# Kernel optimization log

Measured on AMD Instinct MI355X. Metric: run time of the kernel, lower is better.

## Reference

```python
import jax, jax.numpy as jnp
import numpy as np

B, T, E, WIN, OC, VOCAB = 256, 2048, 128, 5, 128, 50000


def setup_inputs() -> dict:
    key = jax.random.key(0)
    k1, k2, k3, k4, k5, k6 = jax.random.split(key, 6)
    return {
        "x": jax.random.randint(k1, (B, T), 0, VOCAB + 1, dtype=jnp.int32),
        "emb_table": jax.random.normal(k2, (VOCAB + 1, E), dtype=jnp.float32),
        "att_w": jax.random.normal(k3, (WIN, E), dtype=jnp.float32) * 0.05,
        "att_b": jax.random.normal(k4, (1,), dtype=jnp.float32),
        "cnn_w": jax.random.normal(k5, (OC, E), dtype=jnp.float32) * 0.05,
        "cnn_b": jax.random.normal(k6, (OC,), dtype=jnp.float32),
    }


def reference(x, emb_table, att_w, att_b, cnn_w, cnn_b):
    win = att_w.shape[0]
    pad = (win - 1) // 2
    embed = emb_table[x]                                   # [B, T, E]
    x_pad = jnp.pad(embed, ((0, 0), (pad, pad), (0, 0)))
    T_ = embed.shape[1]
    # Sliding-window dot product over full embed dim (the degenerate Conv2d)
    s = jnp.zeros(embed.shape[:2], dtype=embed.dtype)      # [B, T]
    for k in range(win):
        s = s + jnp.einsum('bte,e->bt', x_pad[:, k:k + T_, :], att_w[k])
    scores = jax.nn.sigmoid(s + att_b[0])                  # [B, T]
    gated = embed * scores[:, :, None]                     # [B, T, E]
    feat = jnp.tanh(jnp.einsum('bte,oe->bto', gated, cnn_w) + cnn_b)  # [B, T, OC]
    out = jnp.max(feat, axis=1)                            # [B, OC] (maxpool over seq)
    return out[:, :, None, None]                           # [B, OC, 1, 1]
```

## Files before the change

kernel.cpp:

```cpp
#include <hip/hip_runtime.h>
#include <hip/hip_bf16.h>
#include <math.h>

#define B_   256
#define T_   2048
#define E_   128
#define WIN_ 5
#define PAD_ 2
#define OC_  128
#define VOCAB_MAX 50000
#define VOCAB1 50001
#define TT   64
#define REAL_ROWS (TT + WIN_ - 1)
#define ROWS 80
#define ASTR 136
#define VROWS 64

typedef __attribute__((ext_vector_type(8))) short short8;
typedef __attribute__((ext_vector_type(4))) float floatx4;
typedef __attribute__((ext_vector_type(4))) unsigned uintx4;

static __device__ __forceinline__ short f2bf(float f) {
    union { __hip_bfloat16 h; short s; } u;
    u.h = __float2bfloat16(f);
    return u.s;
}

__device__ __forceinline__ void atomicMaxFloat(float* addr, float v) {
    if (v >= 0.0f) atomicMax((int*)addr, __float_as_int(v));
    else           atomicMin((unsigned int*)addr, __float_as_uint(v));
}

__launch_bounds__(256, 4)
__global__ void build_tables(const float* __restrict__ emb,
                             const float* __restrict__ cnn_w,
                             const float* __restrict__ att_w,
                             short* __restrict__ D,
                             float* __restrict__ r,
                             float* __restrict__ out) {
    __shared__ short sh_a[VROWS * ASTR];

    const int tid  = threadIdx.x;
    const int lane = tid & 63;
    const int w    = tid >> 6;
    const int l15  = lane & 15;
    const int quad = lane >> 4;
    const int v0   = blockIdx.x * VROWS;

    if (blockIdx.x < (B_ * OC_) / 256)
        out[blockIdx.x * 256 + tid] = -INFINITY;

    #pragma unroll
    for (int t = 0; t < 8; t++) {
        int i   = t * 256 + tid;
        int row = i >> 5, c4 = i & 31;
        int vr  = v0 + row; if (vr > VOCAB_MAX) vr = VOCAB_MAX;
        float4 v = *(const float4*)(emb + (size_t)vr * E_ + c4 * 4);
        short4 o; o.x = f2bf(v.x); o.y = f2bf(v.y); o.z = f2bf(v.z); o.w = f2bf(v.w);
        *(short4*)(&sh_a[row * ASTR + c4 * 4]) = o;
    }

    short8 Bf[2][4];
    #pragma unroll
    for (int j = 0; j < 2; j++)
        #pragma unroll
        for (int ks = 0; ks < 4; ks++) {
            const float4* p = (const float4*)(cnn_w + (size_t)(w * 32 + j * 16 + l15) * E_ + ks * 32 + quad * 8);
            float4 p0 = p[0], p1 = p[1];
            Bf[j][ks] = (short8){ f2bf(p0.x), f2bf(p0.y), f2bf(p0.z), f2bf(p0.w),
                                  f2bf(p1.x), f2bf(p1.y), f2bf(p1.z), f2bf(p1.w) };
        }

    short8 Ba[4];
    #pragma unroll
    for (int ks = 0; ks < 4; ks++) {
        short8 v = (short8){0,0,0,0,0,0,0,0};
        if (l15 < WIN_) {
            const float4* p = (const float4*)(att_w + (size_t)l15 * E_ + ks * 32 + quad * 8);
            float4 p0 = p[0], p1 = p[1];
            v = (short8){ f2bf(p0.x), f2bf(p0.y), f2bf(p0.z), f2bf(p0.w),
                          f2bf(p1.x), f2bf(p1.y), f2bf(p1.z), f2bf(p1.w) };
        }
        Ba[ks] = v;
    }
    __syncthreads();

    #pragma unroll
    for (int mt = 0; mt < 4; mt++) {
        short8 a[4];
        #pragma unroll
        for (int ks = 0; ks < 4; ks++)
            a[ks] = *(const short8*)(&sh_a[(mt * 16 + l15) * ASTR + ks * 32 + quad * 8]);
        #pragma unroll
        for (int j = 0; j < 2; j++) {
            floatx4 acc = (floatx4){0.f, 0.f, 0.f, 0.f};
            #pragma unroll
            for (int ks = 0; ks < 4; ks++)
                acc = __builtin_amdgcn_mfma_f32_16x16x32_bf16(a[ks], Bf[j][ks], acc, 0, 0, 0);
            #pragma unroll
            for (int rr = 0; rr < 4; rr++) {
                int v = v0 + mt * 16 + quad * 4 + rr;
                if (v <= VOCAB_MAX)
                    D[(size_t)v * E_ + w * 32 + j * 16 + l15] = f2bf(acc[rr]);
            }
        }
    }

    {
        short8 a[4];
        #pragma unroll
        for (int ks = 0; ks < 4; ks++)
            a[ks] = *(const short8*)(&sh_a[(w * 16 + l15) * ASTR + ks * 32 + quad * 8]);
        floatx4 acc = (floatx4){0.f, 0.f, 0.f, 0.f};
        #pragma unroll
        for (int ks = 0; ks < 4; ks++)
            acc = __builtin_amdgcn_mfma_f32_16x16x32_bf16(a[ks], Ba[ks], acc, 0, 0, 0);
        if (l15 < 8) {
            #pragma unroll
            for (int rr = 0; rr < 4; rr++) {
                int v = v0 + w * 16 + quad * 4 + rr;
                if (v <= VOCAB_MAX) r[(size_t)v * 8 + l15] = acc[rr];
            }
        }
    }
}

__launch_bounds__(256, 8)
__global__ void score_max(const int* __restrict__ x,
                          const short* __restrict__ D,
                          const float* __restrict__ r,
                          const float* __restrict__ att_b_p,
                          const float* __restrict__ cnn_b,
                          float* __restrict__ out) {
    __shared__ int   sh_x[260];
    __shared__ float sh_sc[256];
    __shared__ float sh_red[4][128];

    const int tid  = threadIdx.x;
    const int lane = tid & 63;
    const int w    = tid >> 6;
    const int b    = blockIdx.y;
    const int t0   = blockIdx.x * 256;
    const int l15  = lane & 15;
    const int grp  = lane >> 4;

    for (int i = tid; i < 260; i += 256) {
        int t = t0 + i - PAD_;
        sh_x[i] = (t >= 0 && t < T_) ? x[b * T_ + t] : -1;
    }
    __syncthreads();

    {
        float s = att_b_p[0];
        #pragma unroll
        for (int k = 0; k < WIN_; k++) {
            int v = sh_x[tid + k];
            if (v >= 0) s += r[(size_t)v * 8 + k];
        }
        sh_sc[tid] = 1.0f / (1.0f + __expf(-s));
    }
    __syncthreads();

    float mm[8];
    #pragma unroll
    for (int c = 0; c < 8; c++) mm[c] = -INFINITY;

    const int base_t = w * 64;
    for (int i0 = 0; i0 < 64; i0 += 16) {
        uintx4 u[4];
        float  sc4[4];
        #pragma unroll
        for (int j = 0; j < 4; j++) {
            int tok = base_t + i0 + j * 4 + grp;
            int v   = sh_x[tok + PAD_];
            sc4[j]  = sh_sc[tok];
            u[j]    = *(const uintx4*)(D + (size_t)v * E_ + l15 * 8);
        }
        #pragma unroll
        for (int j = 0; j < 4; j++) {
            #pragma unroll
            for (int q = 0; q < 4; q++) {
                float lo = __uint_as_float(u[j][q] << 16);
                float hi = __uint_as_float(u[j][q] & 0xFFFF0000u);
                mm[q * 2]     = fmaxf(mm[q * 2],     sc4[j] * lo);
                mm[q * 2 + 1] = fmaxf(mm[q * 2 + 1], sc4[j] * hi);
            }
        }
    }
    #pragma unroll
    for (int c = 0; c < 8; c++) {
        mm[c] = fmaxf(mm[c], __shfl_xor(mm[c], 16));
        mm[c] = fmaxf(mm[c], __shfl_xor(mm[c], 32));
    }
    if (lane < 16) {
        #pragma unroll
        for (int c = 0; c < 8; c++) sh_red[w][l15 * 8 + c] = mm[c];
    }
    __syncthreads();
    if (tid < 128) {
        float m = fmaxf(fmaxf(sh_red[0][tid], sh_red[1][tid]),
                        fmaxf(sh_red[2][tid], sh_red[3][tid]));
        atomicMaxFloat(&out[b * OC_ + tid], tanhf(m + cnn_b[tid]));
    }
}

__global__ void prep_small(const float* __restrict__ cnn_w, const float* __restrict__ att_w,
                           short* __restrict__ wsw, short* __restrict__ wsatt) {
    int i = blockIdx.x * 256 + threadIdx.x;
    if (i < OC_ * E_)  wsw[i]   = f2bf(cnn_w[i]);
    if (i < WIN_ * E_) wsatt[i] = f2bf(att_w[i]);
}

__launch_bounds__(256, 4)
__global__ void fallback_main(const int* __restrict__ x,
                              const float* __restrict__ emb,
                              const float* __restrict__ att_b_p,
                              const short* __restrict__ wsw,
                              const short* __restrict__ wsatt,
                              const float* __restrict__ cnn_b,
                              float* __restrict__ out) {
    __shared__ short sh_a[ROWS * ASTR];
    __shared__ short sh_att[16 * ASTR];
    __shared__ float sh_r[ROWS * 8];
    __shared__ float sh_score[TT];
    __shared__ int   sh_idx[8 * ROWS];

    const int tid  = threadIdx.x;
    const int lane = tid & 63;
    const int w    = tid >> 6;
    const int b    = blockIdx.y;
    const int t0   = blockIdx.x * (8 * TT);
    const int l15  = lane & 15;
    const int quad = lane >> 4;
    const int rbase = tid >> 4;
    const int c     = tid & 15;

    for (int i = tid; i < 8 * ROWS; i += 256) {
        int tile = i / ROWS, row = i - tile * ROWS;
        int t = t0 + tile * TT + row - PAD_;
        sh_idx[i] = (row < REAL_ROWS && t >= 0 && t < T_) ? x[b * T_ + t] : -1;
    }
    {
        int o = tid >> 4, cc = tid & 15;
        short8 v = (short8){0,0,0,0,0,0,0,0};
        if (o < WIN_) v = *(const short8*)(wsatt + o * E_ + cc * 8);
        *(short8*)(&sh_att[o * ASTR + cc * 8]) = v;
    }
    short8 Bf[2][4];
    #pragma unroll
    for (int j = 0; j < 2; j++)
        #pragma unroll
        for (int ks = 0; ks < 4; ks++)
            Bf[j][ks] = *(const short8*)(wsw + (size_t)(w * 32 + j * 16 + l15) * E_ + ks * 32 + quad * 8);
    __syncthreads();

    short8 g[5];
    #pragma unroll
    for (int k = 0; k < 5; k++) {
        int idx = sh_idx[rbase + 16 * k];
        short8 v = (short8){0,0,0,0,0,0,0,0};
        if (idx >= 0) {
            const float4* p = (const float4*)(emb + (size_t)idx * E_ + c * 8);
            float4 p0 = p[0], p1 = p[1];
            v = (short8){ f2bf(p0.x), f2bf(p0.y), f2bf(p0.z), f2bf(p0.w),
                          f2bf(p1.x), f2bf(p1.y), f2bf(p1.z), f2bf(p1.w) };
        }
        g[k] = v;
    }
    #pragma unroll
    for (int k = 0; k < 5; k++)
        *(short8*)(&sh_a[(rbase + 16 * k) * ASTR + c * 8]) = g[k];
    __syncthreads();

    const float attb = att_b_p[0];
    float mm[2] = { -INFINITY, -INFINITY };

    for (int it = 0; it < 8; it++) {
        for (int mt = w; mt < 5; mt += 4) {
            floatx4 acc = (floatx4){0.f, 0.f, 0.f, 0.f};
            #pragma unroll
            for (int ks = 0; ks < 4; ks++) {
                short8 a  = *(const short8*)(&sh_a[(mt * 16 + l15) * ASTR + ks * 32 + quad * 8]);
                short8 bs = *(const short8*)(&sh_att[l15 * ASTR + ks * 32 + quad * 8]);
                acc = __builtin_amdgcn_mfma_f32_16x16x32_bf16(a, bs, acc, 0, 0, 0);
            }
            if (l15 < 8) {
                #pragma unroll
                for (int r = 0; r < 4; r++)
                    sh_r[(mt * 16 + quad * 4 + r) * 8 + l15] = acc[r];
            }
        }
        __syncthreads();

        if (it + 1 < 8) {
            const int* idxp = &sh_idx[(it + 1) * ROWS];
            #pragma unroll
            for (int k = 0; k < 5; k++) {
                int idx = idxp[rbase + 16 * k];
                short8 v = (short8){0,0,0,0,0,0,0,0};
                if (idx >= 0) {
                    const float4* p = (const float4*)(emb + (size_t)idx * E_ + c * 8);
                    float4 p0 = p[0], p1 = p[1];
                    v = (short8){ f2bf(p0.x), f2bf(p0.y), f2bf(p0.z), f2bf(p0.w),
                                  f2bf(p1.x), f2bf(p1.y), f2bf(p1.z), f2bf(p1.w) };
                }
                g[k] = v;
            }
        }

        if (tid < TT) {
            float s = attb;
            #pragma unroll
            for (int k = 0; k < WIN_; k++) s += sh_r[(tid + k) * 8 + k];
            sh_score[tid] = 1.0f / (1.0f + __expf(-s));
        }

        floatx4 acc[4][2];
        #pragma unroll
        for (int i = 0; i < 4; i++)
            #pragma unroll
            for (int j = 0; j < 2; j++) acc[i][j] = (floatx4){0.f, 0.f, 0.f, 0.f};
        #pragma unroll
        for (int ks = 0; ks < 4; ks++) {
            int ko = ks * 32 + quad * 8;
            #pragma unroll
            for (int i = 0; i < 4; i++) {
                short8 ai = *(const short8*)(&sh_a[(PAD_ + i * 16 + l15) * ASTR + ko]);
                acc[i][0] = __builtin_amdgcn_mfma_f32_16x16x32_bf16(ai, Bf[0][ks], acc[i][0], 0, 0, 0);
                acc[i][1] = __builtin_amdgcn_mfma_f32_16x16x32_bf16(ai, Bf[1][ks], acc[i][1], 0, 0, 0);
            }
        }
        __syncthreads();

        #pragma unroll
        for (int i = 0; i < 4; i++) {
            #pragma unroll
            for (int r = 0; r < 4; r++) {
                float sc = sh_score[i * 16 + quad * 4 + r];
                mm[0] = fmaxf(mm[0], sc * acc[i][0][r]);
                mm[1] = fmaxf(mm[1], sc * acc[i][1][r]);
            }
        }

        if (it + 1 < 8) {
            #pragma unroll
            for (int k = 0; k < 5; k++)
                *(short8*)(&sh_a[(rbase + 16 * k) * ASTR + c * 8]) = g[k];
            __syncthreads();
        }
    }

    #pragma unroll
    for (int j = 0; j < 2; j++) {
        float m = mm[j];
        m = fmaxf(m, __shfl_xor(m, 16));
        m = fmaxf(m, __shfl_xor(m, 32));
        if (lane < 16) {
            int o = w * 32 + j * 16 + lane;
            atomicMaxFloat(&out[b * OC_ + o], tanhf(m + cnn_b[o]));
        }
    }
}

extern "C" void kernel_launch(void* const* d_in, const int* in_sizes, int n_in,
                              void* d_out, int out_size, void* d_ws, size_t ws_size,
                              hipStream_t stream) {
    const int*   x     = (const int*)d_in[0];
    const float* emb   = (const float*)d_in[1];
    const float* att_w = (const float*)d_in[2];
    const float* att_b = (const float*)d_in[3];
    const float* cnn_w = (const float*)d_in[4];
    const float* cnn_b = (const float*)d_in[5];
    float* out = (float*)d_out;

    const size_t d_elems = (size_t)VOCAB1 * E_;
    const size_t r_elems = (size_t)VOCAB1 * 8;
    const size_t need = d_elems * 2 + r_elems * 4 + 64;

    if (ws_size >= need) {
        short* Dt = (short*)d_ws;
        float* rt = (float*)(Dt + d_elems);
        build_tables<<<(VOCAB1 + VROWS - 1) / VROWS, 256, 0, stream>>>(emb, cnn_w, att_w, Dt, rt, out);
        dim3 grid(T_ / 256, B_);
        score_max<<<grid, 256, 0, stream>>>(x, Dt, rt, att_b, cnn_b, out);
    } else {
        hipMemsetAsync(d_out, 0xFF, (size_t)B_ * OC_ * sizeof(float), stream);
        short* ws_w   = (short*)d_ws;
        short* ws_att = ws_w + OC_ * E_;
        prep_small<<<16, 256, 0, stream>>>(cnn_w, att_w, ws_w, ws_att);
        dim3 grid(T_ / (8 * TT), B_);
        fallback_main<<<grid, 256, 0, stream>>>(x, emb, att_b, ws_w, ws_att, cnn_b, out);
    }
}
```

Measured before the change: 119.1 us.

## Split score_max blocks across output-channel quarters to increase parallelism

The score_max grid is expanded fourfold so each block handles one 32-channel slice of the output for its 256-token span. Each lane now gathers one 16-byte chunk of the table row for four tokens, which cuts per-thread loop work and spreads gathers over more wavefronts. The cost is that the window scores (gathers from r plus sigmoid) and the index staging are recomputed in every channel-slice block. There are also four times as many atomics, and the per-row accesses are narrower.

```diff
diff --git a/kernel.cpp b/kernel.cpp
--- a/kernel.cpp
+++ b/kernel.cpp
@@ -134,15 +134,16 @@
                           float* __restrict__ out) {
     __shared__ int   sh_x[260];
     __shared__ float sh_sc[256];
-    __shared__ float sh_red[4][128];
+    __shared__ float sh_red[4][32];
 
     const int tid  = threadIdx.x;
     const int lane = tid & 63;
     const int w    = tid >> 6;
     const int b    = blockIdx.y;
-    const int t0   = blockIdx.x * 256;
-    const int l15  = lane & 15;
-    const int grp  = lane >> 4;
+    const int cc   = blockIdx.x & 3;
+    const int t0   = (blockIdx.x >> 2) * 256;
+    const int lq   = lane & 3;
+    const int lt   = lane >> 2;
 
     for (int i = tid; i < 260; i += 256) {
         int t = t0 + i - PAD_;
@@ -166,41 +167,42 @@
     for (int c = 0; c < 8; c++) mm[c] = -INFINITY;
 
     const int base_t = w * 64;
-    for (int i0 = 0; i0 < 64; i0 += 16) {
-        uintx4 u[4];
-        float  sc4[4];
-        #pragma unroll
-        for (int j = 0; j < 4; j++) {
-            int tok = base_t + i0 + j * 4 + grp;
-            int v   = sh_x[tok + PAD_];
-            sc4[j]  = sh_sc[tok];
-            u[j]    = *(const uintx4*)(D + (size_t)v * E_ + l15 * 8);
-        }
-        #pragma unroll
-        for (int j = 0; j < 4; j++) {
-            #pragma unroll
-            for (int q = 0; q < 4; q++) {
-                float lo = __uint_as_float(u[j][q] << 16);
-                float hi = __uint_as_float(u[j][q] & 0xFFFF0000u);
-                mm[q * 2]     = fmaxf(mm[q * 2],     sc4[j] * lo);
-                mm[q * 2 + 1] = fmaxf(mm[q * 2 + 1], sc4[j] * hi);
-            }
+    uintx4 u[4];
+    float  sc4[4];
+    #pragma unroll
+    for (int g = 0; g < 4; g++) {
+        int tok = base_t + g * 16 + lt;
+        int v   = sh_x[tok + PAD_];
+        sc4[g]  = sh_sc[tok];
+        u[g]    = *(const uintx4*)(D + (size_t)v * E_ + cc * 32 + lq * 8);
+    }
+    #pragma unroll
+    for (int g = 0; g < 4; g++) {
+        #pragma unroll
+        for (int q = 0; q < 4; q++) {
+            float lo = __uint_as_float(u[g][q] << 16);
+            float hi = __uint_as_float(u[g][q] & 0xFFFF0000u);
+            mm[q * 2]     = fmaxf(mm[q * 2],     sc4[g] * lo);
+            mm[q * 2 + 1] = fmaxf(mm[q * 2 + 1], sc4[g] * hi);
         }
     }
     #pragma unroll
     for (int c = 0; c < 8; c++) {
+        mm[c] = fmaxf(mm[c], __shfl_xor(mm[c], 4));
+        mm[c] = fmaxf(mm[c], __shfl_xor(mm[c], 8));
         mm[c] = fmaxf(mm[c], __shfl_xor(mm[c], 16));
         mm[c] = fmaxf(mm[c], __shfl_xor(mm[c], 32));
     }
-    if (lane < 16) {
-        #pragma unroll
-        for (int c = 0; c < 8; c++) sh_red[w][l15 * 8 + c] = mm[c];
-    }
-    __syncthreads();
-    if (tid < 128) {
+    if (lane < 4) {
+        #pragma unroll
+        for (int c = 0; c < 8; c++) sh_red[w][lane * 8 + c] = mm[c];
+    }
+    __syncthreads();
+    if (tid < 32) {
         float m = fmaxf(fmaxf(sh_red[0][tid], sh_red[1][tid]),
                         fmaxf(sh_red[2][tid], sh_red[3][tid]));
-        atomicMaxFloat(&out[b * OC_ + tid], tanhf(m + cnn_b[tid]));
+        int o = cc * 32 + tid;
+        atomicMaxFloat(&out[b * OC_ + o], tanhf(m + cnn_b[o]));
     }
 }
 
@@ -381,7 +383,7 @@
         short* Dt = (short*)d_ws;
         float* rt = (float*)(Dt + d_elems);
         build_tables<<<(VOCAB1 + VROWS - 1) / VROWS, 256, 0, stream>>>(emb, cnn_w, att_w, Dt, rt, out);
-        dim3 grid(T_ / 256, B_);
+        dim3 grid((T_ / 256) * 4, B_);
         score_max<<<grid, 256, 0, stream>>>(x, Dt, rt, att_b, cnn_b, out);
     } else {
         hipMemsetAsync(d_out, 0xFF, (size_t)B_ * OC_ * sizeof(float), stream);
```

Result: slower. 151.0 us (+26.7%).

## Double tokens per block, stage attention table rows in LDS, widen gather batches

Applied to the files above, without the earlier changes.

Each score_max block now covers 512 tokens instead of 256, which halves the grid and halves the per-block atomics and reduction overhead. The per-token attention scalars are now read once per token as a float4 plus one scalar into shared memory, replacing five scattered global reads per token. The D-row gather loop issues 8 loads per batch instead of 4 to expose more memory-level parallelism. The cost is more LDS and registers per block, with the occupancy hint lowered from 8 to 6.

```diff
diff --git a/kernel.cpp b/kernel.cpp
--- a/kernel.cpp
+++ b/kernel.cpp
@@ -15,6 +15,7 @@
 #define ROWS 80
 #define ASTR 136
 #define VROWS 64
+#define BT   512
 
 typedef __attribute__((ext_vector_type(8))) short short8;
 typedef __attribute__((ext_vector_type(4))) float floatx4;
@@ -125,39 +126,55 @@
     }
 }
 
-__launch_bounds__(256, 8)
+__launch_bounds__(256, 6)
 __global__ void score_max(const int* __restrict__ x,
                           const short* __restrict__ D,
                           const float* __restrict__ r,
                           const float* __restrict__ att_b_p,
                           const float* __restrict__ cnn_b,
                           float* __restrict__ out) {
-    __shared__ int   sh_x[260];
-    __shared__ float sh_sc[256];
+    __shared__ int   sh_x[BT + 4];
+    __shared__ float sh_rt[WIN_][BT + 8];
+    __shared__ float sh_sc[BT];
     __shared__ float sh_red[4][128];
 
     const int tid  = threadIdx.x;
     const int lane = tid & 63;
     const int w    = tid >> 6;
     const int b    = blockIdx.y;
-    const int t0   = blockIdx.x * 256;
+    const int t0   = blockIdx.x * BT;
     const int l15  = lane & 15;
     const int grp  = lane >> 4;
 
-    for (int i = tid; i < 260; i += 256) {
+    for (int i = tid; i < BT + 4; i += 256) {
         int t = t0 + i - PAD_;
         sh_x[i] = (t >= 0 && t < T_) ? x[b * T_ + t] : -1;
     }
     __syncthreads();
 
+    for (int i = tid; i < BT + 4; i += 256) {
+        int v = sh_x[i];
+        float4 r03 = make_float4(0.f, 0.f, 0.f, 0.f);
+        float  r4  = 0.f;
+        if (v >= 0) {
+            r03 = *(const float4*)(r + (size_t)v * 8);
+            r4  = r[(size_t)v * 8 + 4];
+        }
+        sh_rt[0][i] = r03.x; sh_rt[1][i] = r03.y; sh_rt[2][i] = r03.z;
+        sh_rt[3][i] = r03.w; sh_rt[4][i] = r4;
+    }
+    __syncthreads();
+
     {
-        float s = att_b_p[0];
-        #pragma unroll
-        for (int k = 0; k < WIN_; k++) {
-            int v = sh_x[tid + k];
-            if (v >= 0) s += r[(size_t)v * 8 + k];
-        }
-        sh_sc[tid] = 1.0f / (1.0f + __expf(-s));
+        const float attb = att_b_p[0];
+        #pragma unroll
+        for (int rep = 0; rep < 2; rep++) {
+            int j = rep * 256 + tid;
+            float s = attb;
+            #pragma unroll
+            for (int k = 0; k < WIN_; k++) s += sh_rt[k][j + k];
+            sh_sc[j] = 1.0f / (1.0f + __expf(-s));
+        }
     }
     __syncthreads();
 
@@ -165,25 +182,26 @@
     #pragma unroll
     for (int c = 0; c < 8; c++) mm[c] = -INFINITY;
 
-    const int base_t = w * 64;
-    for (int i0 = 0; i0 < 64; i0 += 16) {
-        uintx4 u[4];
-        float  sc4[4];
-        #pragma unroll
-        for (int j = 0; j < 4; j++) {
-            int tok = base_t + i0 + j * 4 + grp;
+    const int base_t = w * 128;
+    for (int batch = 0; batch < 4; batch++) {
+        uintx4 u[8];
+        float  sc8[8];
+        const int start = base_t + batch * 32;
+        #pragma unroll
+        for (int j = 0; j < 8; j++) {
+            int tok = start + j * 4 + grp;
             int v   = sh_x[tok + PAD_];
-            sc4[j]  = sh_sc[tok];
+            sc8[j]  = sh_sc[tok];
             u[j]    = *(const uintx4*)(D + (size_t)v * E_ + l15 * 8);
         }
         #pragma unroll
-        for (int j = 0; j < 4; j++) {
+        for (int j = 0; j < 8; j++) {
             #pragma unroll
             for (int q = 0; q < 4; q++) {
                 float lo = __uint_as_float(u[j][q] << 16);
                 float hi = __uint_as_float(u[j][q] & 0xFFFF0000u);
-                mm[q * 2]     = fmaxf(mm[q * 2],     sc4[j] * lo);
-                mm[q * 2 + 1] = fmaxf(mm[q * 2 + 1], sc4[j] * hi);
+                mm[q * 2]     = fmaxf(mm[q * 2],     sc8[j] * lo);
+                mm[q * 2 + 1] = fmaxf(mm[q * 2 + 1], sc8[j] * hi);
             }
         }
     }
@@ -381,7 +399,7 @@
         short* Dt = (short*)d_ws;
         float* rt = (float*)(Dt + d_elems);
         build_tables<<<(VOCAB1 + VROWS - 1) / VROWS, 256, 0, stream>>>(emb, cnn_w, att_w, Dt, rt, out);
-        dim3 grid(T_ / 256, B_);
+        dim3 grid(T_ / BT, B_);
         score_max<<<grid, 256, 0, stream>>>(x, Dt, rt, att_b, cnn_b, out);
     } else {
         hipMemsetAsync(d_out, 0xFF, (size_t)B_ * OC_ * sizeof(float), stream);
```

Measured after the change: 112.0 us (median of 2 runs). -6.0%, faster.
